# Kernel optimization log

Measured on AMD Instinct MI355X. Metric: run time of the kernel, lower is better.

Reference implementation:

```python
import jax, jax.numpy as jnp
import numpy as np

B, T = 1, 600            # batch_size, seq_len (ms)
U = 10                   # n_bkg_units
N_V1, N_LM = 200000, 50000
NNZ_V1, NNZ_LM = 800000, 200000   # neurons * n_bkg_connections(=4)
LAM = 1000.0 / 1000.0    # bkg_units_firing_rate / 1000 -> Poisson rate per ms


def setup_inputs() -> dict:
    key = jax.random.key(0)
    ks = jax.random.split(key, 7)
    inp = jax.random.normal(ks[0], (B, T, 1), dtype=jnp.float32)
    w_v1 = jax.random.normal(ks[1], (NNZ_V1,), dtype=jnp.float32)
    rows_v1 = jax.random.randint(ks[2], (NNZ_V1,), 0, N_V1, dtype=jnp.int32)
    cols_v1 = jax.random.randint(ks[3], (NNZ_V1,), 0, U, dtype=jnp.int32)
    w_lm = jax.random.normal(ks[4], (NNZ_LM,), dtype=jnp.float32)
    rows_lm = jax.random.randint(ks[5], (NNZ_LM,), 0, N_LM, dtype=jnp.int32)
    cols_lm = jax.random.randint(ks[6], (NNZ_LM,), 0, U, dtype=jnp.int32)
    return {"inp": inp, "w_v1": w_v1, "rows_v1": rows_v1, "cols_v1": cols_v1,
            "w_lm": w_lm, "rows_lm": rows_lm, "cols_lm": cols_lm}


def _column_current(spikes, w, rows, cols, n_neurons):
    # Scatter COO weights into a dense (n_neurons, U) matrix (duplicates sum,
    # matching tf.sparse semantics); U is tiny so this is cheap, then a single
    # GEMM reproduces sparse_dense_matmul(W, spikes^T)^T exactly.
    W = jnp.zeros((n_neurons, U), dtype=spikes.dtype).at[rows, cols].add(w)
    i_in = spikes @ W.T                      # (B*T, n_neurons)
    return i_in.reshape(B, T, n_neurons)


def reference(inp, w_v1, rows_v1, cols_v1, w_lm, rows_lm, cols_lm):
    # Poisson background spikes, fixed key for determinism. inp only sets seq_len.
    pkey = jax.random.key(42)
    spikes = jax.random.poisson(pkey, LAM, (B * T, U)).astype(jnp.float32)
    v1 = _column_current(spikes, w_v1, rows_v1, cols_v1, N_V1)   # (B,T,N_V1)
    lm = _column_current(spikes, w_lm, rows_lm, cols_lm, N_LM)   # (B,T,N_LM)
    return jnp.concatenate([v1, lm], axis=-1)                    # (B,T,N_V1+N_LM)
```

## Files before the change

### kernel.cpp

```cpp
#include <hip/hip_runtime.h>
#include <stdint.h>

#define NV1 200000
#define NLM 50000
#define NTOT 250000
#define TLEN 600
#define UU 10
#define NNZV1 800000
#define NNZLM 200000
#define NNZTOT (NNZV1 + NNZLM)
#define NELEM (TLEN * UU)

#define BINSHIFT 9
#define BINROWS 512
#define NB 489
#define SBLK 256
#define SPT 3907

#define WT_OFF        0ULL
#define SPIKES_OFF    10000000ULL
#define BINSTART_OFF  10024000ULL
#define BINCUR_OFF    10026000ULL
#define BINTOT_OFF    10028000ULL
#define SORT_OFF      10030000ULL
#define WS_NEED_SORT  18030000ULL
#define WS_NEED_FALLBACK 10024000ULL

typedef float f32x4 __attribute__((ext_vector_type(4)));
typedef float f32x2 __attribute__((ext_vector_type(2)));
typedef unsigned long long u64;

__device__ __forceinline__ void tf2x32(uint32_t k0, uint32_t k1,
                                       uint32_t c0, uint32_t c1,
                                       uint32_t& o0, uint32_t& o1) {
  const uint32_t ks2 = k0 ^ k1 ^ 0x1BD11BDAu;
  uint32_t x0 = c0 + k0;
  uint32_t x1 = c1 + k1;
#define TF_RND(r) { x0 += x1; x1 = (x1 << (r)) | (x1 >> (32 - (r))); x1 ^= x0; }
  TF_RND(13) TF_RND(15) TF_RND(26) TF_RND(6)
  x0 += k1;  x1 += ks2 + 1u;
  TF_RND(17) TF_RND(29) TF_RND(16) TF_RND(24)
  x0 += ks2; x1 += k0 + 2u;
  TF_RND(13) TF_RND(15) TF_RND(26) TF_RND(6)
  x0 += k0;  x1 += k1 + 3u;
  TF_RND(17) TF_RND(29) TF_RND(16) TF_RND(24)
  x0 += k1;  x1 += ks2 + 4u;
  TF_RND(13) TF_RND(15) TF_RND(26) TF_RND(6)
  x0 += ks2; x1 += k0 + 5u;
#undef TF_RND
  o0 = x0; o1 = x1;
}

__device__ __forceinline__ int spike_value(int e) {
  uint32_t r0 = 0u, r1 = 42u;
  float S = 0.0f;
  int result = 63;
  for (int iter = 0; iter < 64; ++iter) {
    uint32_t n0, n1, s0, s1;
    tf2x32(r0, r1, 0u, 0u, n0, n1);
    tf2x32(r0, r1, 0u, 1u, s0, s1);
    r0 = n0; r1 = n1;
    uint32_t h0, h1;
    tf2x32(s0, s1, 0u, (uint32_t)e, h0, h1);
    const uint32_t bits = h0 ^ h1;
    const float u = __uint_as_float((bits >> 9) | 0x3f800000u) - 1.0f;
    S += logf(u);
    if (!(S > -1.0f)) { result = iter; break; }
  }
  return result;
}

__device__ __forceinline__ void load_nnz(int i,
                                         const float* __restrict__ wv, const int* __restrict__ rv,
                                         const int* __restrict__ cv,
                                         const float* __restrict__ wl, const int* __restrict__ rl,
                                         const int* __restrict__ cl,
                                         int& grow, int& col, float& w) {
  if (i < NNZV1) { grow = rv[i]; col = cv[i]; w = wv[i]; }
  else { const int j = i - NNZV1; grow = NV1 + rl[j]; col = cl[j]; w = wl[j]; }
}

__global__ void __launch_bounds__(256) k1_spikes(float* __restrict__ spikes,
                                                 uint32_t* __restrict__ binTotal) {
  const int gid = blockIdx.x * 256 + threadIdx.x;
  if (gid < NB) binTotal[gid] = 0u;
  if (gid < NELEM) spikes[gid] = (float)spike_value(gid);
}

__global__ void __launch_bounds__(256) k2a_hist(const float* __restrict__ wv, const int* __restrict__ rv,
                                                const int* __restrict__ cv,
                                                const float* __restrict__ wl, const int* __restrict__ rl,
                                                const int* __restrict__ cl,
                                                uint32_t* __restrict__ binTotal) {
  __shared__ uint32_t hist[512];
  const int t = threadIdx.x;
  hist[t] = 0u; hist[t + 256] = 0u;
  __syncthreads();
  const int base = blockIdx.x * SPT;
#pragma unroll
  for (int r = 0; r < 16; ++r) {
    const int il = r * 256 + t;
    const int i = base + il;
    if (il < SPT && i < NNZTOT) {
      int grow, col; float w;
      load_nnz(i, wv, rv, cv, wl, rl, cl, grow, col, w);
      atomicAdd(&hist[grow >> BINSHIFT], 1u);
    }
  }
  __syncthreads();
  uint32_t h0 = hist[t], h1 = (t + 256 < NB) ? hist[t + 256] : 0u;
  if (t < NB && h0) atomicAdd(&binTotal[t], h0);
  if (t + 256 < NB && h1) atomicAdd(&binTotal[t + 256], h1);
}

__global__ void __launch_bounds__(512) k2b_scan(const uint32_t* __restrict__ binTotal,
                                                uint32_t* __restrict__ binstart,
                                                uint32_t* __restrict__ binCursor) {
  __shared__ uint32_t tot[512];
  const int t = threadIdx.x;
  tot[t] = (t < NB) ? binTotal[t] : 0u;
  __syncthreads();
  if (t <= NB) {
    uint32_t s = 0;
    for (int i = 0; i < t && i < NB; ++i) s += tot[i];
    binstart[t] = s;
    if (t < NB) binCursor[t] = s;
  }
}

__global__ void __launch_bounds__(256) k3_reorder(const float* __restrict__ wv, const int* __restrict__ rv,
                                                  const int* __restrict__ cv,
                                                  const float* __restrict__ wl, const int* __restrict__ rl,
                                                  const int* __restrict__ cl,
                                                  uint32_t* __restrict__ binCursor,
                                                  u64* __restrict__ sorted) {
  __shared__ uint32_t hist[512];
  __shared__ uint32_t cur[512];
  const int t = threadIdx.x;
  hist[t] = 0u; hist[t + 256] = 0u;
  __syncthreads();
  const int base = blockIdx.x * SPT;
#pragma unroll
  for (int r = 0; r < 16; ++r) {
    const int il = r * 256 + t;
    const int i = base + il;
    if (il < SPT && i < NNZTOT) {
      int grow, col; float w;
      load_nnz(i, wv, rv, cv, wl, rl, cl, grow, col, w);
      atomicAdd(&hist[grow >> BINSHIFT], 1u);
    }
  }
  __syncthreads();
  for (int b = t; b < NB; b += 256) {
    const uint32_t h = hist[b];
    cur[b] = h ? atomicAdd(&binCursor[b], h) : 0u;
  }
  __syncthreads();
#pragma unroll
  for (int r = 0; r < 16; ++r) {
    const int il = r * 256 + t;
    const int i = base + il;
    if (il < SPT && i < NNZTOT) {
      int grow, col; float w;
      load_nnz(i, wv, rv, cv, wl, rl, cl, grow, col, w);
      const int bin = grow >> BINSHIFT;
      const uint32_t pos = atomicAdd(&cur[bin], 1u);
      const uint32_t rc = (uint32_t)grow | ((uint32_t)col << 18);
      sorted[pos] = ((u64)rc << 32) | (u64)__float_as_uint(w);
    }
  }
}

#define BPB 2
#define K4_BLOCKS ((NB + BPB - 1) / BPB)
__global__ void __launch_bounds__(256) k4_accum(const u64* __restrict__ sorted,
                                                const uint32_t* __restrict__ binstart,
                                                float* __restrict__ WT) {
  __shared__ float acc[BINROWS * BPB * UU];
  const int t = threadIdx.x;
  const int blk = blockIdx.x;
  const int bin0 = blk * BPB;
  const int row0 = bin0 << BINSHIFT;
  for (int i = t; i < BINROWS * BPB * UU; i += 256) acc[i] = 0.f;
  __syncthreads();
  const int lo = (int)binstart[bin0];
  const int hiIdx = (bin0 + BPB < NB) ? (bin0 + BPB) : NB;
  const int hi = (int)binstart[hiIdx];
  for (int i = lo + t; i < hi; i += 256) {
    const u64 v = sorted[i];
    const uint32_t rc = (uint32_t)(v >> 32);
    const float w = __uint_as_float((uint32_t)v);
    const int row = (int)(rc & 0x3FFFFu);
    const int col = (int)(rc >> 18);
    atomicAdd(&acc[(row - row0) * UU + col], w);
  }
  __syncthreads();
#pragma unroll
  for (int u = 0; u < UU; ++u) {
    for (int rbase = 0; rbase < BINROWS * BPB; rbase += 256) {
      const int r = rbase + t;
      const int n = row0 + r;
      if (n < NTOT) WT[(size_t)u * NTOT + n] = acc[r * UU + u];
    }
  }
}

#define WZ4 (NTOT * UU / 4)
#define ZB  ((WZ4 + 255) / 256)
#define SB  ((NELEM + 255) / 256)
__global__ void __launch_bounds__(256) init_kernel(f32x4* __restrict__ W4,
                                                   float* __restrict__ spikes) {
  const int b = blockIdx.x;
  if (b < ZB) {
    const int i = b * 256 + threadIdx.x;
    if (i < WZ4) W4[i] = (f32x4)(0.f);
    return;
  }
  const int e = (b - ZB) * 256 + threadIdx.x;
  if (e >= NELEM) return;
  spikes[e] = (float)spike_value(e);
}

__global__ void scatter_kernel(const float* __restrict__ w_v1,
                               const int* __restrict__ rows_v1,
                               const int* __restrict__ cols_v1,
                               const float* __restrict__ w_lm,
                               const int* __restrict__ rows_lm,
                               const int* __restrict__ cols_lm,
                               float* __restrict__ WT) {
  const int i = blockIdx.x * blockDim.x + threadIdx.x;
  if (i >= NNZTOT) return;
  if (i < NNZV1) {
    atomicAdd(&WT[(size_t)cols_v1[i] * NTOT + rows_v1[i]], w_v1[i]);
  } else {
    const int j = i - NNZV1;
    atomicAdd(&WT[(size_t)cols_lm[j] * NTOT + NV1 + rows_lm[j]], w_lm[j]);
  }
}

#define TTILE 75
#define SROW 12
#define NT4 (NTOT / 4)
__global__ void __launch_bounds__(256, 8) out_kernel(const float* __restrict__ WT,
                                                     const float* __restrict__ spikes,
                                                     float* __restrict__ out) {
  __shared__ float s[TTILE * SROW];
  const int t0 = blockIdx.y * TTILE;
  for (int i = threadIdx.x; i < TTILE * SROW; i += 256) {
    const int row = i / SROW, u = i - row * SROW;
    s[i] = (u < UU) ? spikes[(t0 + row) * UU + u] : 0.f;
  }
  __syncthreads();

  const int n4 = blockIdx.x * 256 + threadIdx.x;
  if (n4 >= NT4) return;
  const int n = n4 * 4;

  f32x4 w[UU];
#pragma unroll
  for (int u = 0; u < UU; ++u)
    w[u] = *reinterpret_cast<const f32x4*>(&WT[(size_t)u * NTOT + n]);

  float* op = &out[(size_t)t0 * NTOT + n];
  for (int t = 0; t < TTILE; ++t) {
    const f32x4 sA = *reinterpret_cast<const f32x4*>(&s[t * SROW]);
    const f32x4 sB = *reinterpret_cast<const f32x4*>(&s[t * SROW + 4]);
    const f32x2 sC = *reinterpret_cast<const f32x2*>(&s[t * SROW + 8]);
    f32x4 acc = sA.x * w[0];
    acc += sA.y * w[1];
    acc += sA.z * w[2];
    acc += sA.w * w[3];
    acc += sB.x * w[4];
    acc += sB.y * w[5];
    acc += sB.z * w[6];
    acc += sB.w * w[7];
    acc += sC.x * w[8];
    acc += sC.y * w[9];
    __builtin_nontemporal_store(acc, reinterpret_cast<f32x4*>(op));
    op += NTOT;
  }
}

extern "C" void kernel_launch(void* const* d_in, const int* in_sizes, int n_in,
                              void* d_out, int out_size, void* d_ws, size_t ws_size,
                              hipStream_t stream) {
  const float* w_v1    = (const float*)d_in[1];
  const int*   rows_v1 = (const int*)d_in[2];
  const int*   cols_v1 = (const int*)d_in[3];
  const float* w_lm    = (const float*)d_in[4];
  const int*   rows_lm = (const int*)d_in[5];
  const int*   cols_lm = (const int*)d_in[6];
  float* out = (float*)d_out;

  char* ws = (char*)d_ws;
  float*    WT        = (float*)(ws + WT_OFF);
  float*    spikes    = (float*)(ws + SPIKES_OFF);
  uint32_t* binstart  = (uint32_t*)(ws + BINSTART_OFF);
  uint32_t* binCursor = (uint32_t*)(ws + BINCUR_OFF);
  uint32_t* binTotal  = (uint32_t*)(ws + BINTOT_OFF);
  u64*      sorted    = (u64*)(ws + SORT_OFF);

  if (ws_size >= WS_NEED_SORT) {
    k1_spikes<<<SB, 256, 0, stream>>>(spikes, binTotal);
    k2a_hist<<<SBLK, 256, 0, stream>>>(w_v1, rows_v1, cols_v1,
                                       w_lm, rows_lm, cols_lm, binTotal);
    k2b_scan<<<1, 512, 0, stream>>>(binTotal, binstart, binCursor);
    k3_reorder<<<SBLK, 256, 0, stream>>>(w_v1, rows_v1, cols_v1,
                                         w_lm, rows_lm, cols_lm, binCursor, sorted);
    k4_accum<<<K4_BLOCKS, 256, 0, stream>>>(sorted, binstart, WT);
  } else if (ws_size >= WS_NEED_FALLBACK) {
    init_kernel<<<ZB + SB, 256, 0, stream>>>((f32x4*)WT, spikes);
    scatter_kernel<<<(NNZTOT + 255) / 256, 256, 0, stream>>>(w_v1, rows_v1, cols_v1,
                                                             w_lm, rows_lm, cols_lm, WT);
  } else {
    return;
  }

  dim3 grid((NT4 + 255) / 256, TLEN / TTILE);
  out_kernel<<<grid, 256, 0, stream>>>(WT, spikes, out);
}
```

Measured before the change: 181.8 us.

## Fuse bin accumulation with output GEMM and trim histogram loads

Replaces the accumulate-to-WT kernel plus the separate output kernel with one fused kernel. Each block accumulates its bin rows in LDS, then streams all 600 timesteps of output directly using register-held weights and nontemporal stores. The histogram kernel now loads only row indices instead of the full COO triplets. This removes the dense WT round trip and one launch, but it runs the output write with far fewer blocks and a large LDS footprint, which risks lower occupancy and reduced write bandwidth.

```diff
diff --git a/kernel.cpp b/kernel.cpp
--- a/kernel.cpp
+++ b/kernel.cpp
@@ -80,6 +80,12 @@
   else { const int j = i - NNZV1; grow = NV1 + rl[j]; col = cl[j]; w = wl[j]; }
 }
 
+__device__ __forceinline__ int load_row(int i,
+                                        const int* __restrict__ rv,
+                                        const int* __restrict__ rl) {
+  return (i < NNZV1) ? rv[i] : (NV1 + rl[i - NNZV1]);
+}
+
 __global__ void __launch_bounds__(256) k1_spikes(float* __restrict__ spikes,
                                                  uint32_t* __restrict__ binTotal) {
   const int gid = blockIdx.x * 256 + threadIdx.x;
@@ -87,10 +93,8 @@
   if (gid < NELEM) spikes[gid] = (float)spike_value(gid);
 }
 
-__global__ void __launch_bounds__(256) k2a_hist(const float* __restrict__ wv, const int* __restrict__ rv,
-                                                const int* __restrict__ cv,
-                                                const float* __restrict__ wl, const int* __restrict__ rl,
-                                                const int* __restrict__ cl,
+__global__ void __launch_bounds__(256) k2a_hist(const int* __restrict__ rv,
+                                                const int* __restrict__ rl,
                                                 uint32_t* __restrict__ binTotal) {
   __shared__ uint32_t hist[512];
   const int t = threadIdx.x;
@@ -101,11 +105,8 @@
   for (int r = 0; r < 16; ++r) {
     const int il = r * 256 + t;
     const int i = base + il;
-    if (il < SPT && i < NNZTOT) {
-      int grow, col; float w;
-      load_nnz(i, wv, rv, cv, wl, rl, cl, grow, col, w);
-      atomicAdd(&hist[grow >> BINSHIFT], 1u);
-    }
+    if (il < SPT && i < NNZTOT)
+      atomicAdd(&hist[load_row(i, rv, rl) >> BINSHIFT], 1u);
   }
   __syncthreads();
   uint32_t h0 = hist[t], h1 = (t + 256 < NB) ? hist[t + 256] : 0u;
@@ -144,11 +145,8 @@
   for (int r = 0; r < 16; ++r) {
     const int il = r * 256 + t;
     const int i = base + il;
-    if (il < SPT && i < NNZTOT) {
-      int grow, col; float w;
-      load_nnz(i, wv, rv, cv, wl, rl, cl, grow, col, w);
-      atomicAdd(&hist[grow >> BINSHIFT], 1u);
-    }
+    if (il < SPT && i < NNZTOT)
+      atomicAdd(&hist[load_row(i, rv, rl) >> BINSHIFT], 1u);
   }
   __syncthreads();
   for (int b = t; b < NB; b += 256) {
@@ -172,17 +170,26 @@
 }
 
 #define BPB 2
-#define K4_BLOCKS ((NB + BPB - 1) / BPB)
-__global__ void __launch_bounds__(256) k4_accum(const u64* __restrict__ sorted,
+#define K5_BLOCKS ((NB + BPB - 1) / BPB)
+#define K5_ACC (BINROWS * BPB * UU)
+#define SROW 12
+__global__ void __launch_bounds__(256) k5_fused(const u64* __restrict__ sorted,
                                                 const uint32_t* __restrict__ binstart,
-                                                float* __restrict__ WT) {
-  __shared__ float acc[BINROWS * BPB * UU];
+                                                const float* __restrict__ spikes,
+                                                float* __restrict__ out) {
+  __shared__ float acc[K5_ACC];
+  __shared__ float s[TLEN * SROW];
   const int t = threadIdx.x;
-  const int blk = blockIdx.x;
-  const int bin0 = blk * BPB;
+  const int bin0 = blockIdx.x * BPB;
   const int row0 = bin0 << BINSHIFT;
-  for (int i = t; i < BINROWS * BPB * UU; i += 256) acc[i] = 0.f;
-  __syncthreads();
+
+  for (int i = t; i < K5_ACC; i += 256) acc[i] = 0.f;
+  for (int i = t; i < TLEN * SROW; i += 256) {
+    const int row = i / SROW, u = i - row * SROW;
+    s[i] = (u < UU) ? spikes[row * UU + u] : 0.f;
+  }
+  __syncthreads();
+
   const int lo = (int)binstart[bin0];
   const int hiIdx = (bin0 + BPB < NB) ? (bin0 + BPB) : NB;
   const int hi = (int)binstart[hiIdx];
@@ -190,18 +197,41 @@
     const u64 v = sorted[i];
     const uint32_t rc = (uint32_t)(v >> 32);
     const float w = __uint_as_float((uint32_t)v);
-    const int row = (int)(rc & 0x3FFFFu);
-    const int col = (int)(rc >> 18);
-    atomicAdd(&acc[(row - row0) * UU + col], w);
-  }
-  __syncthreads();
-#pragma unroll
-  for (int u = 0; u < UU; ++u) {
-    for (int rbase = 0; rbase < BINROWS * BPB; rbase += 256) {
-      const int r = rbase + t;
-      const int n = row0 + r;
-      if (n < NTOT) WT[(size_t)u * NTOT + n] = acc[r * UU + u];
+    atomicAdd(&acc[((int)(rc & 0x3FFFFu) - row0) * UU + (int)(rc >> 18)], w);
+  }
+  __syncthreads();
+
+  const int n = row0 + t * 4;
+  if (n >= NTOT) return;
+  float w[4][UU];
+#pragma unroll
+  for (int r = 0; r < 4; ++r)
+#pragma unroll
+    for (int u = 0; u < UU; ++u)
+      w[r][u] = acc[(t * 4 + r) * UU + u];
+
+  float* op = out + n;
+  for (int tt = 0; tt < TLEN; ++tt) {
+    const f32x4 sA = *reinterpret_cast<const f32x4*>(&s[tt * SROW]);
+    const f32x4 sB = *reinterpret_cast<const f32x4*>(&s[tt * SROW + 4]);
+    const f32x2 sC = *reinterpret_cast<const f32x2*>(&s[tt * SROW + 8]);
+    f32x4 a;
+#pragma unroll
+    for (int r = 0; r < 4; ++r) {
+      float x = sA.x * w[r][0];
+      x = fmaf(sA.y, w[r][1], x);
+      x = fmaf(sA.z, w[r][2], x);
+      x = fmaf(sA.w, w[r][3], x);
+      x = fmaf(sB.x, w[r][4], x);
+      x = fmaf(sB.y, w[r][5], x);
+      x = fmaf(sB.z, w[r][6], x);
+      x = fmaf(sB.w, w[r][7], x);
+      x = fmaf(sC.x, w[r][8], x);
+      x = fmaf(sC.y, w[r][9], x);
+      a[r] = x;
     }
+    __builtin_nontemporal_store(a, reinterpret_cast<f32x4*>(op));
+    op += NTOT;
   }
 }
 
@@ -239,7 +269,6 @@
 }
 
 #define TTILE 75
-#define SROW 12
 #define NT4 (NTOT / 4)
 __global__ void __launch_bounds__(256, 8) out_kernel(const float* __restrict__ WT,
                                                      const float* __restrict__ spikes,
@@ -302,20 +331,16 @@
 
   if (ws_size >= WS_NEED_SORT) {
     k1_spikes<<<SB, 256, 0, stream>>>(spikes, binTotal);
-    k2a_hist<<<SBLK, 256, 0, stream>>>(w_v1, rows_v1, cols_v1,
-                                       w_lm, rows_lm, cols_lm, binTotal);
+    k2a_hist<<<SBLK, 256, 0, stream>>>(rows_v1, rows_lm, binTotal);
     k2b_scan<<<1, 512, 0, stream>>>(binTotal, binstart, binCursor);
     k3_reorder<<<SBLK, 256, 0, stream>>>(w_v1, rows_v1, cols_v1,
                                          w_lm, rows_lm, cols_lm, binCursor, sorted);
-    k4_accum<<<K4_BLOCKS, 256, 0, stream>>>(sorted, binstart, WT);
+    k5_fused<<<K5_BLOCKS, 256, 0, stream>>>(sorted, binstart, spikes, out);
   } else if (ws_size >= WS_NEED_FALLBACK) {
     init_kernel<<<ZB + SB, 256, 0, stream>>>((f32x4*)WT, spikes);
     scatter_kernel<<<(NNZTOT + 255) / 256, 256, 0, stream>>>(w_v1, rows_v1, cols_v1,
                                                              w_lm, rows_lm, cols_lm, WT);
-  } else {
-    return;
-  }
-
-  dim3 grid((NT4 + 255) / 256, TLEN / TTILE);
-  out_kernel<<<grid, 256, 0, stream>>>(WT, spikes, out);
-}
+    dim3 grid((NT4 + 255) / 256, TLEN / TTILE);
+    out_kernel<<<grid, 256, 0, stream>>>(WT, spikes, out);
+  }
+}
```

Result: faster. 174.1 us (-4.3%).
